# Performance work log

Hardware: AMD Instinct MI355X
Metric: run time of the kernel (lower is better)

Reference implementation:

```python
import jax, jax.numpy as jnp
import numpy as np

B, T, D, H, L, O = 256, 512, 64, 256, 2, 4


def _lstm_layer(x_tbd, W_ih, W_hh, b_ih, b_hh):
    """x_tbd: (T, B, D_in) -> hidden sequence (T, B, H). PyTorch gate order i,f,g,o."""
    Bb = x_tbd.shape[1]
    Hh = W_hh.shape[1]
    b = b_ih + b_hh
    # precompute input projections for all timesteps in one GEMM
    xW = jnp.einsum('tbd,gd->tbg', x_tbd, W_ih) + b  # (T, B, 4H)

    def step(carry, xw_t):
        h, c = carry
        gates = xw_t + h @ W_hh.T
        i, f, g, o = jnp.split(gates, 4, axis=-1)
        i = jax.nn.sigmoid(i)
        f = jax.nn.sigmoid(f)
        g = jnp.tanh(g)
        o = jax.nn.sigmoid(o)
        c = f * c + i * g
        h = o * jnp.tanh(c)
        return (h, c), h

    init = (jnp.zeros((Bb, Hh), x_tbd.dtype), jnp.zeros((Bb, Hh), x_tbd.dtype))
    _, hs = jax.lax.scan(step, init, xW)
    return hs


def setup_inputs() -> dict:
    key = jax.random.key(0)
    ks = jax.random.split(key, 11)
    s = 1.0 / np.sqrt(H)  # PyTorch LSTM init scale
    inp = {
        'x': jax.random.normal(ks[0], (B, T, D), dtype=jnp.float32),
        'W_ih0': jax.random.uniform(ks[1], (4 * H, D), minval=-s, maxval=s, dtype=jnp.float32),
        'W_hh0': jax.random.uniform(ks[2], (4 * H, H), minval=-s, maxval=s, dtype=jnp.float32),
        'b_ih0': jax.random.uniform(ks[3], (4 * H,), minval=-s, maxval=s, dtype=jnp.float32),
        'b_hh0': jax.random.uniform(ks[4], (4 * H,), minval=-s, maxval=s, dtype=jnp.float32),
        'W_ih1': jax.random.uniform(ks[5], (4 * H, H), minval=-s, maxval=s, dtype=jnp.float32),
        'W_hh1': jax.random.uniform(ks[6], (4 * H, H), minval=-s, maxval=s, dtype=jnp.float32),
        'b_ih1': jax.random.uniform(ks[7], (4 * H,), minval=-s, maxval=s, dtype=jnp.float32),
        'b_hh1': jax.random.uniform(ks[8], (4 * H,), minval=-s, maxval=s, dtype=jnp.float32),
        'fc_W': jax.random.uniform(ks[9], (O, H), minval=-s, maxval=s, dtype=jnp.float32),
        'fc_b': jax.random.uniform(ks[10], (O,), minval=-s, maxval=s, dtype=jnp.float32),
    }
    return inp


def reference(x, W_ih0, W_hh0, b_ih0, b_hh0, W_ih1, W_hh1, b_ih1, b_hh1, fc_W, fc_b):
    xt = jnp.transpose(x, (1, 0, 2))            # (T, B, D), batch_first -> time-major
    h1 = _lstm_layer(xt, W_ih0, W_hh0, b_ih0, b_hh0)   # (T, B, H)
    h2 = _lstm_layer(h1, W_ih1, W_hh1, b_ih1, b_hh1)   # (T, B, H)
    last = h2[-1]                                # out[:, -1, :] in batch_first layout
    return last @ fc_W.T + fc_b                  # (B, O)
```

## Files before the change

kernel.cpp:

```cpp
#include <hip/hip_runtime.h>


#define TT 512
#define HH 256
#define DD 64

typedef __attribute__((ext_vector_type(2))) _Float16 h2t;
typedef __attribute__((ext_vector_type(8))) _Float16 f16x8;
typedef __attribute__((ext_vector_type(4))) float f32x4;
typedef unsigned long long u64;
typedef unsigned u32;

__device__ __forceinline__ u32 pkh(float x, float y) {
    h2t h; h.x = (_Float16)x; h.y = (_Float16)y;
    return __builtin_bit_cast(u32, h);
}
__device__ __forceinline__ float sigf(float x) { return 1.f / (1.f + __expf(-x)); }
__device__ __forceinline__ float tanhf_(float x) {
    float e = __expf(2.f * x);
    return 1.f - 2.f / (e + 1.f);
}
__device__ __forceinline__ f16x8 ld8(const float* p) {
    float4 u = ((const float4*)p)[0];
    float4 v = ((const float4*)p)[1];
    f16x8 r = {(_Float16)u.x, (_Float16)u.y, (_Float16)u.z, (_Float16)u.w,
               (_Float16)v.x, (_Float16)v.y, (_Float16)v.z, (_Float16)v.w};
    return r;
}
__device__ __forceinline__ u32 ld32(const u32* p) {
    return __hip_atomic_load(p, __ATOMIC_RELAXED, __HIP_MEMORY_SCOPE_AGENT);
}
__device__ __forceinline__ void st32(u32* p, u32 v) {
    __hip_atomic_store(p, v, __ATOMIC_RELAXED, __HIP_MEMORY_SCOPE_AGENT);
}
__device__ __forceinline__ u64 ld64(const u64* p) {
    return __hip_atomic_load(p, __ATOMIC_RELAXED, __HIP_MEMORY_SCOPE_AGENT);
}
__device__ __forceinline__ void st64(u64* p, u64 v) {
    __hip_atomic_store(p, v, __ATOMIC_RELAXED, __HIP_MEMORY_SCOPE_AGENT);
}

__global__ __launch_bounds__(512, 2) void lstm_persist(
    const float* __restrict__ x,
    const float* __restrict__ Wih0, const float* __restrict__ Whh0,
    const float* __restrict__ bih0, const float* __restrict__ bhh0,
    const float* __restrict__ Wih1, const float* __restrict__ Whh1,
    const float* __restrict__ bih1, const float* __restrict__ bhh1,
    const float* __restrict__ fcW, const float* __restrict__ fcb,
    float* __restrict__ out,
    u64* h0ring, u64* h1ring, u32* cflagsA)
{
    __shared__ __align__(16) _Float16 sB[9216];
    __shared__ __align__(16) float part2[2][8][276];

    const int tid  = threadIdx.x;
    const int g    = blockIdx.x & 31;
    const int role = blockIdx.x >> 5;
    const bool isL1 = role >= 4;
    const int q = role & 3;
    const int batch0 = g * 8;
    u64* ring0 = h0ring + (size_t)g * 4096;
    u64* ring1 = h1ring + (size_t)g * 4096;
    u32* cflag = cflagsA + (size_t)g * 16;

    const int lane = tid & 63, w = tid >> 6;
    const int mw = w & 3, kh = w >> 2;
    const int bcol = lane & 15, kc = lane >> 4;

    const int R0 = mw * 256 + 64 * q + (lane & 15);
    const int R1 = R0 + 16, R2 = R0 + 32, R3 = R0 + 48;

#define DECL_TI(ti) f16x8 A##ti##_0={},A##ti##_1={},A##ti##_2={},A##ti##_3={}, \
                          A##ti##_4={},A##ti##_5={},A##ti##_6={},A##ti##_7={};
    DECL_TI(0) DECL_TI(1) DECL_TI(2) DECL_TI(3)
#undef DECL_TI

    if (isL1) {
#define LDA1(ti,j) { int k_ = (kh*8+(j))*32 + kc*8;                          \
        A##ti##_##j = ld8(k_ < 256 ? Wih1 + (size_t)R##ti*256 + k_           \
                                   : Whh1 + (size_t)R##ti*256 + (k_-256)); }
#define LDA1T(ti) LDA1(ti,0) LDA1(ti,1) LDA1(ti,2) LDA1(ti,3) \
                  LDA1(ti,4) LDA1(ti,5) LDA1(ti,6) LDA1(ti,7)
        LDA1T(0) LDA1T(1) LDA1T(2) LDA1T(3)
#undef LDA1T
#undef LDA1
    } else {
#define LDA0(ti,j) { int k_ = (kh*5+(j))*32 + kc*8;                          \
        A##ti##_##j = ld8(k_ < 64 ? Wih0 + (size_t)R##ti*64 + k_             \
                                  : Whh0 + (size_t)R##ti*256 + (k_-64)); }
#define LDA0T(ti) LDA0(ti,0) LDA0(ti,1) LDA0(ti,2) LDA0(ti,3) LDA0(ti,4)
        LDA0T(0) LDA0T(1) LDA0T(2) LDA0T(3)
#undef LDA0T
#undef LDA0
    }

    const float* bA = isL1 ? bih1 : bih0;
    const float* bB = isL1 ? bhh1 : bhh0;
    const float bz0 = bA[      64*q + lane] + bB[      64*q + lane];
    const float bz1 = bA[256 + 64*q + lane] + bB[256 + 64*q + lane];
    const float bz2 = bA[512 + 64*q + lane] + bB[512 + 64*q + lane];
    const float bz3 = bA[768 + 64*q + lane] + bB[768 + 64*q + lane];
    float cst = 0.f;

    u32* const sBu = (u32*)sB;
    for (int i = tid; i < 4608; i += 512) sBu[i] = 0;

    auto stage_next = [&](int snext) {
        const bool st0 = (!isL1) && (snext < TT);
        const bool st1 = isL1 && (snext >= 1) && (snext <= TT);
        if (!(st0 || st1)) return;
        {
            const int slot = (snext - 1) & 3;
            const u32 e0 = (u32)snext;
            const int base = isL1 ? 0 : 8;
#pragma unroll
            for (int pp = 0; pp < 2; ++pp) {
                int p = tid + pp * 512;
                int j = p >> 7, n = p & 127;
                const u64* a = ring0 + slot * 1024 + (n >> 5) * 256 + j * 32 + (n & 31);
                u64 v;
                do { v = ld64(a); } while ((u32)(v >> 32) != e0);
                sBu[(base + (n >> 2)) * 72 + j * 4 + (n & 3)] = (u32)v;
            }
        }
        if (isL1) {
            const int slot = (snext + 2) & 3;
            const u32 e1 = (snext >= 2) ? (u32)snext : 0u;
#pragma unroll
            for (int pp = 0; pp < 2; ++pp) {
                int p = tid + pp * 512;
                int j = p >> 7, n = p & 127;
                const u64* a = ring1 + slot * 1024 + (n >> 5) * 256 + j * 32 + (n & 31);
                u64 v;
                do { v = ld64(a); } while ((u32)(v >> 32) != e1);
                sBu[(32 + (n >> 2)) * 72 + j * 4 + (n & 3)] = (u32)v;
            }
        } else if (tid >= 256 && tid < 384) {
            int t2 = tid - 256, j = t2 >> 4, c = t2 & 15;
            float4 v = ((const float4*)(x + ((size_t)(batch0 + j) * TT + snext) * DD))[c];
            int bidx = (c >> 1) * 72 + j * 4 + (c & 1) * 2;
            sBu[bidx]     = pkh(v.x, v.y);
            sBu[bidx + 1] = pkh(v.z, v.w);
        }
    };
    stage_next(0);

    for (int s = 0; s <= TT; ++s) {
        __syncthreads();
        if (tid == 0) st32(&cflag[role], (u32)(s + 1));

        const bool act_ = isL1 ? (s >= 1) : (s < TT);

        u32 cpre = 0xFFFFFFFFu;
        if (act_ && lane < 8) cpre = ld32(&cflag[lane]);

        if (act_) {
            f32x4 C0 = {0,0,0,0}, C1 = {0,0,0,0}, C2 = {0,0,0,0}, C3 = {0,0,0,0};
#define MST(j, ktb) { const f16x8 Bf = *(const f16x8*)(sB + (((ktb)+(j))*4 + kc)*144 + bcol*8); \
            C0 = __builtin_amdgcn_mfma_f32_16x16x32_f16(A0_##j, Bf, C0, 0,0,0); \
            C1 = __builtin_amdgcn_mfma_f32_16x16x32_f16(A1_##j, Bf, C1, 0,0,0); \
            C2 = __builtin_amdgcn_mfma_f32_16x16x32_f16(A2_##j, Bf, C2, 0,0,0); \
            C3 = __builtin_amdgcn_mfma_f32_16x16x32_f16(A3_##j, Bf, C3, 0,0,0); }
            if (isL1) {
                const int ktb = kh * 8;
                MST(0,ktb) MST(1,ktb) MST(2,ktb) MST(3,ktb)
                MST(4,ktb) MST(5,ktb) MST(6,ktb) MST(7,ktb)
            } else {
                const int ktb = kh * 5;
                MST(0,ktb) MST(1,ktb) MST(2,ktb) MST(3,ktb) MST(4,ktb)
            }
#undef MST
            if (bcol < 8) {
                *(f32x4*)&part2[kh][bcol][mw*64 +  0 + kc*4] = C0;
                *(f32x4*)&part2[kh][bcol][mw*64 + 16 + kc*4] = C1;
                *(f32x4*)&part2[kh][bcol][mw*64 + 32 + kc*4] = C2;
                *(f32x4*)&part2[kh][bcol][mw*64 + 48 + kc*4] = C3;
            }
        }
        __syncthreads();

        if (act_) {
            float s0 = part2[0][w][      lane] + part2[1][w][      lane] + bz0;
            float s1 = part2[0][w][ 64 + lane] + part2[1][w][ 64 + lane] + bz1;
            float s2 = part2[0][w][128 + lane] + part2[1][w][128 + lane] + bz2;
            float s3 = part2[0][w][192 + lane] + part2[1][w][192 + lane] + bz3;
            float fi = sigf(s0), ff = sigf(s1), fg = tanhf_(s2), fo = sigf(s3);
            cst = ff * cst + fi * fg;
            float h = fo * tanhf_(cst);
            float hn = __shfl_down(h, 1);

            const int tgt = s - 2;
            while (!__all(lane >= 8 || (int)cpre >= tgt)) {
                __builtin_amdgcn_s_sleep(1);
                if (lane < 8) cpre = ld32(&cflag[lane]);
            }
            if (!(lane & 1)) {
                u64 v = ((u64)(u32)(s + 1) << 32) | (u64)pkh(h, hn);
                u64* dst = (isL1 ? ring1 + (size_t)((s - 1) & 3) * 1024
                                 : ring0 + (size_t)(s & 3) * 1024)
                           + q * 256 + w * 32 + (lane >> 1);
                st64(dst, v);
            }
        }

        stage_next(s + 1);
    }

    if (isL1 && q == 0) {
        const u32 ef = (u32)(TT + 1);
#pragma unroll
        for (int pp = 0; pp < 2; ++pp) {
            int p = tid + pp * 512;
            int j = p >> 7, n = p & 127;
            const u64* a = ring1 + 3 * 1024 + (n >> 5) * 256 + j * 32 + (n & 31);
            u64 v;
            do { v = ld64(a); } while ((u32)(v >> 32) != ef);
            sBu[j * 128 + n] = (u32)v;
        }
        __syncthreads();
        const int j = tid >> 6, l2 = tid & 63;
        const int o = l2 >> 4, kk = l2 & 15;
        float ssum = 0.f;
#pragma unroll
        for (int m = 0; m < 16; ++m) {
            int k = kk * 16 + m;
            ssum += (float)sB[j * 256 + k] * fcW[o * HH + k];
        }
#pragma unroll
        for (int off = 8; off; off >>= 1) ssum += __shfl_down(ssum, off);
        if (kk == 0) out[(batch0 + j) * 4 + o] = ssum + fcb[o];
    }
}

extern "C" void kernel_launch(void* const* d_in, const int* in_sizes, int n_in,
                              void* d_out, int out_size, void* d_ws, size_t ws_size,
                              hipStream_t stream)
{
    (void)in_sizes; (void)n_in; (void)out_size; (void)ws_size;
    const float* x    = (const float*)d_in[0];
    const float* Wih0 = (const float*)d_in[1];
    const float* Whh0 = (const float*)d_in[2];
    const float* bih0 = (const float*)d_in[3];
    const float* bhh0 = (const float*)d_in[4];
    const float* Wih1 = (const float*)d_in[5];
    const float* Whh1 = (const float*)d_in[6];
    const float* bih1 = (const float*)d_in[7];
    const float* bhh1 = (const float*)d_in[8];
    const float* fcW  = (const float*)d_in[9];
    const float* fcb  = (const float*)d_in[10];
    float* out = (float*)d_out;

    u64* h0ring = (u64*)d_ws;
    u64* h1ring = (u64*)((char*)d_ws + 1048576);
    u32* cflags = (u32*)((char*)d_ws + 2097152);

    hipMemsetAsync(d_ws, 0, 2097152 + 2048, stream);

    lstm_persist<<<dim3(256), dim3(512), 0, stream>>>(
        x, Wih0, Whh0, bih0, bhh0, Wih1, Whh1, bih1, bhh1, fcW, fcb, out,
        h0ring, h1ring, cflags);
}
```

Measured before the change: 1.278 ms.

## Prefetch ring loads before MFMA and write own hidden slice directly to LDS

Each step now issues the global ring-buffer loads for the next step's hidden state, and the x load, before the MFMA work so their latency overlaps with compute. The spin-wait polling moves after compute and handles all four loads together. Each block writes its own quarter of h straight into shared memory and no longer reads it back from the global ring, which removes some global traffic. The cost is more live registers and trickier ordering: an early speculative load may return stale data and has to be polled again.

```diff
diff --git a/kernel.cpp b/kernel.cpp
--- a/kernel.cpp
+++ b/kernel.cpp
@@ -66,6 +66,11 @@
     const int lane = tid & 63, w = tid >> 6;
     const int mw = w & 3, kh = w >> 2;
     const int bcol = lane & 15, kc = lane >> 4;
+
+    const int n_ = tid & 127;
+    const int jA = tid >> 7;
+    const int jB = 4 + (tid >> 7);
+    const int nq = n_ >> 5;
 
     const int R0 = mw * 256 + 64 * q + (lane & 15);
     const int R1 = R0 + 16, R2 = R0 + 32, R3 = R0 + 48;
@@ -104,55 +109,54 @@
 
     u32* const sBu = (u32*)sB;
     for (int i = tid; i < 4608; i += 512) sBu[i] = 0;
-
-    auto stage_next = [&](int snext) {
-        const bool st0 = (!isL1) && (snext < TT);
-        const bool st1 = isL1 && (snext >= 1) && (snext <= TT);
-        if (!(st0 || st1)) return;
-        {
-            const int slot = (snext - 1) & 3;
-            const u32 e0 = (u32)snext;
-            const int base = isL1 ? 0 : 8;
-#pragma unroll
-            for (int pp = 0; pp < 2; ++pp) {
-                int p = tid + pp * 512;
-                int j = p >> 7, n = p & 127;
-                const u64* a = ring0 + slot * 1024 + (n >> 5) * 256 + j * 32 + (n & 31);
-                u64 v;
-                do { v = ld64(a); } while ((u32)(v >> 32) != e0);
-                sBu[(base + (n >> 2)) * 72 + j * 4 + (n & 3)] = (u32)v;
-            }
-        }
-        if (isL1) {
-            const int slot = (snext + 2) & 3;
-            const u32 e1 = (snext >= 2) ? (u32)snext : 0u;
-#pragma unroll
-            for (int pp = 0; pp < 2; ++pp) {
-                int p = tid + pp * 512;
-                int j = p >> 7, n = p & 127;
-                const u64* a = ring1 + slot * 1024 + (n >> 5) * 256 + j * 32 + (n & 31);
-                u64 v;
-                do { v = ld64(a); } while ((u32)(v >> 32) != e1);
-                sBu[(32 + (n >> 2)) * 72 + j * 4 + (n & 3)] = (u32)v;
-            }
-        } else if (tid >= 256 && tid < 384) {
-            int t2 = tid - 256, j = t2 >> 4, c = t2 & 15;
-            float4 v = ((const float4*)(x + ((size_t)(batch0 + j) * TT + snext) * DD))[c];
-            int bidx = (c >> 1) * 72 + j * 4 + (c & 1) * 2;
-            sBu[bidx]     = pkh(v.x, v.y);
-            sBu[bidx + 1] = pkh(v.z, v.w);
-        }
-    };
-    stage_next(0);
+    __syncthreads();
+
+    if (!isL1 && tid >= 256 && tid < 384) {
+        int t2 = tid - 256, j = t2 >> 4, c = t2 & 15;
+        float4 v = ((const float4*)(x + ((size_t)(batch0 + j) * TT) * DD))[c];
+        int bidx = (c >> 1) * 72 + j * 4 + (c & 1) * 2;
+        sBu[bidx]     = pkh(v.x, v.y);
+        sBu[bidx + 1] = pkh(v.z, v.w);
+    }
 
     for (int s = 0; s <= TT; ++s) {
         __syncthreads();
         if (tid == 0) st32(&cflag[role], (u32)(s + 1));
 
         const bool act_ = isL1 ? (s >= 1) : (s < TT);
+        const int  snx  = s + 1;
+        const bool stg0 = (!isL1) && (snx < TT);
+        const bool stg1 = isL1 && (snx <= TT);
 
         u32 cpre = 0xFFFFFFFFu;
         if (act_ && lane < 8) cpre = ld32(&cflag[lane]);
+
+        u64 v0A = 0, v0B = 0, v1A = 0, v1B = 0;
+        bool k0A = true, k0B = true, k1A = true, k1B = true;
+        const u64 *p0A = nullptr, *p0B = nullptr, *p1A = nullptr, *p1B = nullptr;
+        if (stg0 || stg1) {
+            if (!(!isL1 && nq == q)) {
+                const u64* b0 = ring0 + (size_t)((snx - 1) & 3) * 1024
+                                + (nq << 8) + (n_ & 31);
+                p0A = b0 + jA * 32; p0B = b0 + jB * 32;
+                v0A = ld64(p0A); v0B = ld64(p0B);
+                k0A = false; k0B = false;
+            }
+            if (stg1 && !(nq == q && snx >= 2)) {
+                const u64* b1 = ring1 + (size_t)((snx + 2) & 3) * 1024
+                                + (nq << 8) + (n_ & 31);
+                p1A = b1 + jA * 32; p1B = b1 + jB * 32;
+                v1A = ld64(p1A); v1B = ld64(p1B);
+                k1A = false; k1B = false;
+            }
+        }
+        float4 xreg;
+        const bool doX = stg0 && (tid >= 256) && (tid < 384);
+        if (doX) {
+            int t2 = tid - 256, j = t2 >> 4, c = t2 & 15;
+            xreg = ((const float4*)(x + ((size_t)(batch0 + j) * TT + snx) * DD))[c];
+        }
+        __builtin_amdgcn_sched_barrier(0);
 
         if (act_) {
             f32x4 C0 = {0,0,0,0}, C1 = {0,0,0,0}, C2 = {0,0,0,0}, C3 = {0,0,0,0};
@@ -188,6 +192,13 @@
             cst = ff * cst + fi * fg;
             float h = fo * tanhf_(cst);
             float hn = __shfl_down(h, 1);
+            u32 hw = pkh(h, hn);
+
+            if (!(lane & 1)) {
+                int nn = (64 * q + lane) >> 1;
+                int base = isL1 ? 32 : 8;
+                sBu[(base + (nn >> 2)) * 72 + w * 4 + (nn & 3)] = hw;
+            }
 
             const int tgt = s - 2;
             while (!__all(lane >= 8 || (int)cpre >= tgt)) {
@@ -195,7 +206,7 @@
                 if (lane < 8) cpre = ld32(&cflag[lane]);
             }
             if (!(lane & 1)) {
-                u64 v = ((u64)(u32)(s + 1) << 32) | (u64)pkh(h, hn);
+                u64 v = ((u64)(u32)(s + 1) << 32) | (u64)hw;
                 u64* dst = (isL1 ? ring1 + (size_t)((s - 1) & 3) * 1024
                                  : ring0 + (size_t)(s & 3) * 1024)
                            + q * 256 + w * 32 + (lane >> 1);
@@ -203,7 +214,36 @@
             }
         }
 
-        stage_next(s + 1);
+        if (stg0 || stg1) {
+            const u32 e0 = (u32)snx;
+            const u32 e1 = (snx >= 2) ? (u32)snx : 0u;
+            for (;;) {
+                if (!k0A && (u32)(v0A >> 32) == e0) k0A = true;
+                if (!k0B && (u32)(v0B >> 32) == e0) k0B = true;
+                if (!k1A && (u32)(v1A >> 32) == e1) k1A = true;
+                if (!k1B && (u32)(v1B >> 32) == e1) k1B = true;
+                if (k0A & k0B & k1A & k1B) break;
+                if (!k0A) v0A = ld64(p0A);
+                if (!k0B) v0B = ld64(p0B);
+                if (!k1A) v1A = ld64(p1A);
+                if (!k1B) v1B = ld64(p1B);
+            }
+            if (p0A) {
+                const int base = isL1 ? 0 : 8;
+                sBu[(base + (n_ >> 2)) * 72 + jA * 4 + (n_ & 3)] = (u32)v0A;
+                sBu[(base + (n_ >> 2)) * 72 + jB * 4 + (n_ & 3)] = (u32)v0B;
+            }
+            if (p1A) {
+                sBu[(32 + (n_ >> 2)) * 72 + jA * 4 + (n_ & 3)] = (u32)v1A;
+                sBu[(32 + (n_ >> 2)) * 72 + jB * 4 + (n_ & 3)] = (u32)v1B;
+            }
+            if (doX) {
+                int t2 = tid - 256, j = t2 >> 4, c = t2 & 15;
+                int bidx = (c >> 1) * 72 + j * 4 + (c & 1) * 2;
+                sBu[bidx]     = pkh(xreg.x, xreg.y);
+                sBu[bidx + 1] = pkh(xreg.z, xreg.w);
+            }
+        }
     }
 
     if (isL1 && q == 0) {
```

After: 1.428 ms. 1.12x slower.

## Drop K-split reduction, double-buffer hidden state, write own slice locally

Applied to the files above, without the earlier changes.

Each block now runs 256 threads, and each wave owns the full K range, holding 16 (layer 1) or 10 (layer 0) A fragments per gate in registers. This removes the cross-wave partial-sum exchange through shared memory and one __syncthreads per step. Gate activations are computed directly from MFMA accumulators. The block's own new h slice is written straight into a double-buffered shared tile, so only the other three quarter-blocks' slices are polled from the global ring, with all polls issued before waiting. The cost is much higher register pressure from 64 A fragments per thread in layer 1, and fewer threads per block to hide latency.

```diff
diff --git a/kernel.cpp b/kernel.cpp
--- a/kernel.cpp
+++ b/kernel.cpp
@@ -40,7 +40,7 @@
     __hip_atomic_store(p, v, __ATOMIC_RELAXED, __HIP_MEMORY_SCOPE_AGENT);
 }
 
-__global__ __launch_bounds__(512, 2) void lstm_persist(
+__global__ __launch_bounds__(256, 1) void lstm_persist(
     const float* __restrict__ x,
     const float* __restrict__ Wih0, const float* __restrict__ Whh0,
     const float* __restrict__ bih0, const float* __restrict__ bhh0,
@@ -50,8 +50,8 @@
     float* __restrict__ out,
     u64* h0ring, u64* h1ring, u32* cflagsA)
 {
-    __shared__ __align__(16) _Float16 sB[9216];
-    __shared__ __align__(16) float part2[2][8][276];
+    __shared__ __align__(16) _Float16 sB[18432];
+    __shared__ __align__(16) float sBias[4][64];
 
     const int tid  = threadIdx.x;
     const int g    = blockIdx.x & 31;
@@ -64,170 +64,215 @@
     u32* cflag = cflagsA + (size_t)g * 16;
 
     const int lane = tid & 63, w = tid >> 6;
-    const int mw = w & 3, kh = w >> 2;
-    const int bcol = lane & 15, kc = lane >> 4;
-
-    const int R0 = mw * 256 + 64 * q + (lane & 15);
-    const int R1 = R0 + 16, R2 = R0 + 32, R3 = R0 + 48;
-
-#define DECL_TI(ti) f16x8 A##ti##_0={},A##ti##_1={},A##ti##_2={},A##ti##_3={}, \
-                          A##ti##_4={},A##ti##_5={},A##ti##_6={},A##ti##_7={};
-    DECL_TI(0) DECL_TI(1) DECL_TI(2) DECL_TI(3)
-#undef DECL_TI
+    const int bcol = lane & 15;
+    const int p_   = lane >> 4;
+    const int koff = p_ * 8;
+
+    const int rb = 64 * q + 16 * w + bcol;
+    const int R0 = rb, R1 = 256 + rb, R2 = 512 + rb, R3 = 768 + rb;
+
+#define DECLG(gg) f16x8 A##gg##_0={},A##gg##_1={},A##gg##_2={},A##gg##_3={}, \
+    A##gg##_4={},A##gg##_5={},A##gg##_6={},A##gg##_7={},A##gg##_8={},        \
+    A##gg##_9={},A##gg##_10={},A##gg##_11={},A##gg##_12={},A##gg##_13={},    \
+    A##gg##_14={},A##gg##_15={};
+    DECLG(0) DECLG(1) DECLG(2) DECLG(3)
+#undef DECLG
 
     if (isL1) {
-#define LDA1(ti,j) { int k_ = (kh*8+(j))*32 + kc*8;                          \
-        A##ti##_##j = ld8(k_ < 256 ? Wih1 + (size_t)R##ti*256 + k_           \
-                                   : Whh1 + (size_t)R##ti*256 + (k_-256)); }
-#define LDA1T(ti) LDA1(ti,0) LDA1(ti,1) LDA1(ti,2) LDA1(ti,3) \
-                  LDA1(ti,4) LDA1(ti,5) LDA1(ti,6) LDA1(ti,7)
-        LDA1T(0) LDA1T(1) LDA1T(2) LDA1T(3)
-#undef LDA1T
-#undef LDA1
+#define L1G(gg) \
+    A##gg##_0 =ld8(Wih1+(size_t)R##gg*256+  0+koff); A##gg##_1 =ld8(Wih1+(size_t)R##gg*256+ 32+koff); \
+    A##gg##_2 =ld8(Wih1+(size_t)R##gg*256+ 64+koff); A##gg##_3 =ld8(Wih1+(size_t)R##gg*256+ 96+koff); \
+    A##gg##_4 =ld8(Wih1+(size_t)R##gg*256+128+koff); A##gg##_5 =ld8(Wih1+(size_t)R##gg*256+160+koff); \
+    A##gg##_6 =ld8(Wih1+(size_t)R##gg*256+192+koff); A##gg##_7 =ld8(Wih1+(size_t)R##gg*256+224+koff); \
+    A##gg##_8 =ld8(Whh1+(size_t)R##gg*256+  0+koff); A##gg##_9 =ld8(Whh1+(size_t)R##gg*256+ 32+koff); \
+    A##gg##_10=ld8(Whh1+(size_t)R##gg*256+ 64+koff); A##gg##_11=ld8(Whh1+(size_t)R##gg*256+ 96+koff); \
+    A##gg##_12=ld8(Whh1+(size_t)R##gg*256+128+koff); A##gg##_13=ld8(Whh1+(size_t)R##gg*256+160+koff); \
+    A##gg##_14=ld8(Whh1+(size_t)R##gg*256+192+koff); A##gg##_15=ld8(Whh1+(size_t)R##gg*256+224+koff);
+        L1G(0) L1G(1) L1G(2) L1G(3)
+#undef L1G
     } else {
-#define LDA0(ti,j) { int k_ = (kh*5+(j))*32 + kc*8;                          \
-        A##ti##_##j = ld8(k_ < 64 ? Wih0 + (size_t)R##ti*64 + k_             \
-                                  : Whh0 + (size_t)R##ti*256 + (k_-64)); }
-#define LDA0T(ti) LDA0(ti,0) LDA0(ti,1) LDA0(ti,2) LDA0(ti,3) LDA0(ti,4)
-        LDA0T(0) LDA0T(1) LDA0T(2) LDA0T(3)
-#undef LDA0T
-#undef LDA0
-    }
-
-    const float* bA = isL1 ? bih1 : bih0;
-    const float* bB = isL1 ? bhh1 : bhh0;
-    const float bz0 = bA[      64*q + lane] + bB[      64*q + lane];
-    const float bz1 = bA[256 + 64*q + lane] + bB[256 + 64*q + lane];
-    const float bz2 = bA[512 + 64*q + lane] + bB[512 + 64*q + lane];
-    const float bz3 = bA[768 + 64*q + lane] + bB[768 + 64*q + lane];
-    float cst = 0.f;
-
-    u32* const sBu = (u32*)sB;
-    for (int i = tid; i < 4608; i += 512) sBu[i] = 0;
-
-    auto stage_next = [&](int snext) {
-        const bool st0 = (!isL1) && (snext < TT);
-        const bool st1 = isL1 && (snext >= 1) && (snext <= TT);
-        if (!(st0 || st1)) return;
-        {
-            const int slot = (snext - 1) & 3;
-            const u32 e0 = (u32)snext;
-            const int base = isL1 ? 0 : 8;
-#pragma unroll
-            for (int pp = 0; pp < 2; ++pp) {
-                int p = tid + pp * 512;
-                int j = p >> 7, n = p & 127;
-                const u64* a = ring0 + slot * 1024 + (n >> 5) * 256 + j * 32 + (n & 31);
-                u64 v;
-                do { v = ld64(a); } while ((u32)(v >> 32) != e0);
-                sBu[(base + (n >> 2)) * 72 + j * 4 + (n & 3)] = (u32)v;
-            }
-        }
-        if (isL1) {
-            const int slot = (snext + 2) & 3;
-            const u32 e1 = (snext >= 2) ? (u32)snext : 0u;
-#pragma unroll
-            for (int pp = 0; pp < 2; ++pp) {
-                int p = tid + pp * 512;
-                int j = p >> 7, n = p & 127;
-                const u64* a = ring1 + slot * 1024 + (n >> 5) * 256 + j * 32 + (n & 31);
-                u64 v;
-                do { v = ld64(a); } while ((u32)(v >> 32) != e1);
-                sBu[(32 + (n >> 2)) * 72 + j * 4 + (n & 3)] = (u32)v;
-            }
-        } else if (tid >= 256 && tid < 384) {
-            int t2 = tid - 256, j = t2 >> 4, c = t2 & 15;
-            float4 v = ((const float4*)(x + ((size_t)(batch0 + j) * TT + snext) * DD))[c];
-            int bidx = (c >> 1) * 72 + j * 4 + (c & 1) * 2;
-            sBu[bidx]     = pkh(v.x, v.y);
-            sBu[bidx + 1] = pkh(v.z, v.w);
-        }
-    };
-    stage_next(0);
+#define L0G(gg) \
+    A##gg##_0=ld8(Wih0+(size_t)R##gg*64+koff); A##gg##_1=ld8(Wih0+(size_t)R##gg*64+32+koff); \
+    A##gg##_2=ld8(Whh0+(size_t)R##gg*256+  0+koff); A##gg##_3=ld8(Whh0+(size_t)R##gg*256+ 32+koff); \
+    A##gg##_4=ld8(Whh0+(size_t)R##gg*256+ 64+koff); A##gg##_5=ld8(Whh0+(size_t)R##gg*256+ 96+koff); \
+    A##gg##_6=ld8(Whh0+(size_t)R##gg*256+128+koff); A##gg##_7=ld8(Whh0+(size_t)R##gg*256+160+koff); \
+    A##gg##_8=ld8(Whh0+(size_t)R##gg*256+192+koff); A##gg##_9=ld8(Whh0+(size_t)R##gg*256+224+koff);
+        L0G(0) L0G(1) L0G(2) L0G(3)
+#undef L0G
+    }
+
+    {
+        int g_ = tid >> 6, i_ = tid & 63;
+        const float* bA = isL1 ? bih1 : bih0;
+        const float* bB = isL1 ? bhh1 : bhh0;
+        sBias[g_][i_] = bA[g_ * 256 + 64 * q + i_] + bB[g_ * 256 + 64 * q + i_];
+    }
+    for (int i = tid; i < 9216; i += 256) ((u32*)sB)[i] = 0;
+    __syncthreads();
+    if (!isL1 && tid < 128) {
+        int j = tid >> 4, c = tid & 15;
+        float4 v = ((const float4*)(x + (size_t)(batch0 + j) * TT * DD))[c];
+        int bi = (c >> 1) * 72 + j * 4 + 2 * (c & 1);
+        ((u32*)sB)[bi] = pkh(v.x, v.y); ((u32*)sB)[bi + 1] = pkh(v.z, v.w);
+    }
+
+    float c0_ = 0.f, c1_ = 0.f, c2_ = 0.f, c3_ = 0.f;
 
     for (int s = 0; s <= TT; ++s) {
+        const int par = s & 1;
         __syncthreads();
         if (tid == 0) st32(&cflag[role], (u32)(s + 1));
 
         const bool act_ = isL1 ? (s >= 1) : (s < TT);
-
-        u32 cpre = 0xFFFFFFFFu;
+        const int  snx  = s + 1;
+        const bool stg0 = (!isL1) && (snx < TT);
+        const bool stg1 = isL1 && (snx <= TT);
+
+        u32 cpre = 0u;
         if (act_ && lane < 8) cpre = ld32(&cflag[lane]);
+        float4 xr;
+        const bool doX = stg0 && (tid < 128);
+        if (doX) {
+            int j = tid >> 4, c = tid & 15;
+            xr = ((const float4*)(x + ((size_t)(batch0 + j) * TT + snx) * DD))[c];
+        }
 
         if (act_) {
+            const _Float16* sBp = sB + par * 9216;
             f32x4 C0 = {0,0,0,0}, C1 = {0,0,0,0}, C2 = {0,0,0,0}, C3 = {0,0,0,0};
-#define MST(j, ktb) { const f16x8 Bf = *(const f16x8*)(sB + (((ktb)+(j))*4 + kc)*144 + bcol*8); \
-            C0 = __builtin_amdgcn_mfma_f32_16x16x32_f16(A0_##j, Bf, C0, 0,0,0); \
-            C1 = __builtin_amdgcn_mfma_f32_16x16x32_f16(A1_##j, Bf, C1, 0,0,0); \
-            C2 = __builtin_amdgcn_mfma_f32_16x16x32_f16(A2_##j, Bf, C2, 0,0,0); \
-            C3 = __builtin_amdgcn_mfma_f32_16x16x32_f16(A3_##j, Bf, C3, 0,0,0); }
+#define MST(kt) { const f16x8 Bf = *(const f16x8*)(sBp + ((kt)*4 + p_)*144 + bcol*8); \
+            C0 = __builtin_amdgcn_mfma_f32_16x16x32_f16(A0_##kt, Bf, C0, 0,0,0); \
+            C1 = __builtin_amdgcn_mfma_f32_16x16x32_f16(A1_##kt, Bf, C1, 0,0,0); \
+            C2 = __builtin_amdgcn_mfma_f32_16x16x32_f16(A2_##kt, Bf, C2, 0,0,0); \
+            C3 = __builtin_amdgcn_mfma_f32_16x16x32_f16(A3_##kt, Bf, C3, 0,0,0); }
             if (isL1) {
-                const int ktb = kh * 8;
-                MST(0,ktb) MST(1,ktb) MST(2,ktb) MST(3,ktb)
-                MST(4,ktb) MST(5,ktb) MST(6,ktb) MST(7,ktb)
+                MST(0) MST(1) MST(2) MST(3) MST(4) MST(5) MST(6) MST(7)
+                MST(8) MST(9) MST(10) MST(11) MST(12) MST(13) MST(14) MST(15)
             } else {
-                const int ktb = kh * 5;
-                MST(0,ktb) MST(1,ktb) MST(2,ktb) MST(3,ktb) MST(4,ktb)
+                MST(0) MST(1) MST(2) MST(3) MST(4) MST(5) MST(6) MST(7) MST(8) MST(9)
             }
 #undef MST
             if (bcol < 8) {
-                *(f32x4*)&part2[kh][bcol][mw*64 +  0 + kc*4] = C0;
-                *(f32x4*)&part2[kh][bcol][mw*64 + 16 + kc*4] = C1;
-                *(f32x4*)&part2[kh][bcol][mw*64 + 32 + kc*4] = C2;
-                *(f32x4*)&part2[kh][bcol][mw*64 + 48 + kc*4] = C3;
-            }
-        }
+                const f32x4 bi0 = *(const f32x4*)&sBias[0][16 * w + 4 * p_];
+                const f32x4 bi1 = *(const f32x4*)&sBias[1][16 * w + 4 * p_];
+                const f32x4 bi2 = *(const f32x4*)&sBias[2][16 * w + 4 * p_];
+                const f32x4 bi3 = *(const f32x4*)&sBias[3][16 * w + 4 * p_];
+                float h0v, h1v, h2v, h3v;
+#define ACTR(r, cr) { float fi = sigf(C0[r] + bi0[r]), ff = sigf(C1[r] + bi1[r]); \
+                float fg = tanhf_(C2[r] + bi2[r]), fo = sigf(C3[r] + bi3[r]);     \
+                cr = ff * cr + fi * fg; h##r##v = fo * tanhf_(cr); }
+                ACTR(0, c0_) ACTR(1, c1_) ACTR(2, c2_) ACTR(3, c3_)
+#undef ACTR
+                u32 lo = pkh(h0v, h1v), hi = pkh(h2v, h3v);
+
+                const int idx0 = 64 * q + 16 * w + 4 * p_;
+                u32* dstP = (u32*)sB + (par ^ 1) * 4608;
+                const int sl = ((isL1 ? 32 : 8) + (idx0 >> 3)) * 72 + bcol * 4
+                               + ((idx0 & 7) >> 1);
+                dstP[sl] = lo; dstP[sl + 1] = hi;
+
+                const int tgt = s - 2;
+                while (!__all(lane >= 8 || (int)cpre >= tgt)) {
+                    __builtin_amdgcn_s_sleep(1);
+                    if (lane < 8) cpre = ld32(&cflag[lane]);
+                }
+                const u64 ep = (u64)(u32)(s + 1) << 32;
+                u64* rdst = (isL1 ? ring1 + (size_t)((s - 1) & 3) * 1024
+                                  : ring0 + (size_t)(s & 3) * 1024)
+                            + q * 256 + bcol * 32 + 8 * w + 2 * p_;
+                st64(rdst, ep | (u64)lo);
+                st64(rdst + 1, ep | (u64)hi);
+            }
+        }
+
+        if (stg1) {
+            const int i0 = (q + 1) & 3, i1 = (q + 2) & 3, i2 = (q + 3) & 3;
+            const u64* a0 = ring0 + (size_t)((snx - 1) & 3) * 1024 + tid;
+            const u64* a1 = ring1 + (size_t)((snx + 2) & 3) * 1024 + tid;
+            u64 v0 = ld64(a0),          v1 = ld64(a0 + 256);
+            u64 v2 = ld64(a0 + 512),    v3 = ld64(a0 + 768);
+            u64 v4 = ld64(a1 + i0*256), v5 = ld64(a1 + i1*256), v6 = ld64(a1 + i2*256);
+            const u32 e0 = (u32)snx, e1 = (snx >= 2) ? (u32)snx : 0u;
+            for (;;) {
+                bool k0 = ((u32)(v0 >> 32) == e0), k1 = ((u32)(v1 >> 32) == e0),
+                     k2 = ((u32)(v2 >> 32) == e0), k3 = ((u32)(v3 >> 32) == e0),
+                     k4 = ((u32)(v4 >> 32) == e1), k5 = ((u32)(v5 >> 32) == e1),
+                     k6 = ((u32)(v6 >> 32) == e1);
+                if (k0 & k1 & k2 & k3 & k4 & k5 & k6) break;
+                if (!k0) v0 = ld64(a0);          if (!k1) v1 = ld64(a0 + 256);
+                if (!k2) v2 = ld64(a0 + 512);    if (!k3) v3 = ld64(a0 + 768);
+                if (!k4) v4 = ld64(a1 + i0*256); if (!k5) v5 = ld64(a1 + i1*256);
+                if (!k6) v6 = ld64(a1 + i2*256);
+            }
+            u32* d = (u32*)sB + (par ^ 1) * 4608;
+            const int b = tid >> 5, hp = tid & 31;
+            const int wof = (hp >> 2) * 72 + b * 4 + (hp & 3);
+            d[wof]          = (u32)v0;
+            d[wof + 576]    = (u32)v1;
+            d[wof + 1152]   = (u32)v2;
+            d[wof + 1728]   = (u32)v3;
+            d[wof + 2304 + 576 * i0] = (u32)v4;
+            d[wof + 2304 + 576 * i1] = (u32)v5;
+            d[wof + 2304 + 576 * i2] = (u32)v6;
+        } else if (stg0) {
+            const int i0 = (q + 1) & 3, i1 = (q + 2) & 3, i2 = (q + 3) & 3;
+            const u64* a0 = ring0 + (size_t)((snx - 1) & 3) * 1024 + tid;
+            u64 v0 = ld64(a0 + i0*256), v1 = ld64(a0 + i1*256), v2 = ld64(a0 + i2*256);
+            const u32 e0 = (u32)snx;
+            for (;;) {
+                bool k0 = ((u32)(v0 >> 32) == e0), k1 = ((u32)(v1 >> 32) == e0),
+                     k2 = ((u32)(v2 >> 32) == e0);
+                if (k0 & k1 & k2) break;
+                if (!k0) v0 = ld64(a0 + i0*256);
+                if (!k1) v1 = ld64(a0 + i1*256);
+                if (!k2) v2 = ld64(a0 + i2*256);
+            }
+            u32* d = (u32*)sB + (par ^ 1) * 4608;
+            const int b = tid >> 5, hp = tid & 31;
+            const int wof = (hp >> 2) * 72 + b * 4 + (hp & 3);
+            d[wof + 576 + 576 * i0] = (u32)v0;
+            d[wof + 576 + 576 * i1] = (u32)v1;
+            d[wof + 576 + 576 * i2] = (u32)v2;
+            if (doX) {
+                int j = tid >> 4, c = tid & 15;
+                int bi = (c >> 1) * 72 + j * 4 + 2 * (c & 1);
+                d[bi] = pkh(xr.x, xr.y); d[bi + 1] = pkh(xr.z, xr.w);
+            }
+        }
+    }
+
+    if (role == 4) {
         __syncthreads();
-
-        if (act_) {
-            float s0 = part2[0][w][      lane] + part2[1][w][      lane] + bz0;
-            float s1 = part2[0][w][ 64 + lane] + part2[1][w][ 64 + lane] + bz1;
-            float s2 = part2[0][w][128 + lane] + part2[1][w][128 + lane] + bz2;
-            float s3 = part2[0][w][192 + lane] + part2[1][w][192 + lane] + bz3;
-            float fi = sigf(s0), ff = sigf(s1), fg = tanhf_(s2), fo = sigf(s3);
-            cst = ff * cst + fi * fg;
-            float h = fo * tanhf_(cst);
-            float hn = __shfl_down(h, 1);
-
-            const int tgt = s - 2;
-            while (!__all(lane >= 8 || (int)cpre >= tgt)) {
-                __builtin_amdgcn_s_sleep(1);
-                if (lane < 8) cpre = ld32(&cflag[lane]);
-            }
-            if (!(lane & 1)) {
-                u64 v = ((u64)(u32)(s + 1) << 32) | (u64)pkh(h, hn);
-                u64* dst = (isL1 ? ring1 + (size_t)((s - 1) & 3) * 1024
-                                 : ring0 + (size_t)(s & 3) * 1024)
-                           + q * 256 + w * 32 + (lane >> 1);
-                st64(dst, v);
-            }
-        }
-
-        stage_next(s + 1);
-    }
-
-    if (isL1 && q == 0) {
         const u32 ef = (u32)(TT + 1);
-#pragma unroll
-        for (int pp = 0; pp < 2; ++pp) {
-            int p = tid + pp * 512;
-            int j = p >> 7, n = p & 127;
-            const u64* a = ring1 + 3 * 1024 + (n >> 5) * 256 + j * 32 + (n & 31);
-            u64 v;
-            do { v = ld64(a); } while ((u32)(v >> 32) != ef);
-            sBu[j * 128 + n] = (u32)v;
+        const u64* a = ring1 + 3 * 1024 + tid;
+        u64 w0 = ld64(a), w1 = ld64(a + 256), w2 = ld64(a + 512), w3 = ld64(a + 768);
+        for (;;) {
+            bool k0 = ((u32)(w0 >> 32) == ef), k1 = ((u32)(w1 >> 32) == ef),
+                 k2 = ((u32)(w2 >> 32) == ef), k3 = ((u32)(w3 >> 32) == ef);
+            if (k0 & k1 & k2 & k3) break;
+            if (!k0) w0 = ld64(a);        if (!k1) w1 = ld64(a + 256);
+            if (!k2) w2 = ld64(a + 512);  if (!k3) w3 = ld64(a + 768);
+        }
+        {
+            const int b = tid >> 5, hp = tid & 31;
+            u32* d = (u32*)sB;
+            d[b * 128 + hp]      = (u32)w0;
+            d[b * 128 + 32 + hp] = (u32)w1;
+            d[b * 128 + 64 + hp] = (u32)w2;
+            d[b * 128 + 96 + hp] = (u32)w3;
         }
         __syncthreads();
-        const int j = tid >> 6, l2 = tid & 63;
-        const int o = l2 >> 4, kk = l2 & 15;
+        const int j = tid >> 5, l2 = tid & 31;
+        const int o = l2 >> 3, kk = l2 & 7;
         float ssum = 0.f;
 #pragma unroll
-        for (int m = 0; m < 16; ++m) {
-            int k = kk * 16 + m;
+        for (int m = 0; m < 32; ++m) {
+            int k = kk * 32 + m;
             ssum += (float)sB[j * 256 + k] * fcW[o * HH + k];
         }
-#pragma unroll
-        for (int off = 8; off; off >>= 1) ssum += __shfl_down(ssum, off);
+        ssum += __shfl_down(ssum, 4);
+        ssum += __shfl_down(ssum, 2);
+        ssum += __shfl_down(ssum, 1);
         if (kk == 0) out[(batch0 + j) * 4 + o] = ssum + fcb[o];
     }
 }
@@ -256,7 +301,7 @@
 
     hipMemsetAsync(d_ws, 0, 2097152 + 2048, stream);
 
-    lstm_persist<<<dim3(256), dim3(512), 0, stream>>>(
+    lstm_persist<<<dim3(256), dim3(256), 0, stream>>>(
         x, Wih0, Whh0, bih0, bhh0, Wih1, Whh1, bih1, bhh1, fcW, fcb, out,
         h0ring, h1ring, cflags);
 }
```

Result: slower. 1.667 ms (+30.4%).
